# Optimization experiments

Hardware: AMD Instinct MI355X
Metric: run time of the kernel (lower is better)

Reference implementation:

```python
import jax, jax.numpy as jnp
import numpy as np

B, IN, X, OUT, Z = 4096, 1024, 2048, 512, 6
RES = [False, False, 1, False, 3, False]  # residual_in from init_kwargs
KEEP_P = 0.5  # y: Bernoulli keep-probability for connectivity mask


def _masked_normal(kw, km, shape):
    w = jax.random.normal(kw, shape, dtype=jnp.float32)
    m = jax.random.bernoulli(km, KEEP_P, shape).astype(jnp.float32)
    return w * m


def setup_inputs() -> dict:
    key = jax.random.key(0)
    ks = jax.random.split(key, 40)
    inp = {}
    inp['x'] = jax.random.normal(ks[0], (B, IN), dtype=jnp.float32)
    # weights stored as (in, out) == torch weight.T; mask baked in as in apply_connectivity()
    inp['W_in'] = _masked_normal(ks[1], ks[2], (IN, X))
    inp['b_in'] = jax.random.normal(ks[3], (X,), dtype=jnp.float32)
    hidden_in = [2 * X if RES[i] is not False else X for i in range(Z)]
    for i in range(Z):
        inp[f'Wh{i}'] = _masked_normal(ks[4 + 2 * i], ks[5 + 2 * i], (hidden_in[i], X))
    inp['bh'] = jax.random.normal(ks[20], (Z, X), dtype=jnp.float32)
    inp['W_out'] = _masked_normal(ks[21], ks[22], (X, OUT))
    inp['b_out'] = jax.random.normal(ks[23], (OUT,), dtype=jnp.float32)
    # per-column clip maxima: Poisson(rate=10) as in RandomActivation
    inp['mo_in'] = jax.random.poisson(ks[24], 10.0, (X,)).astype(jnp.float32)
    inp['mo_h'] = jax.random.poisson(ks[25], 10.0, (Z, X)).astype(jnp.float32)
    inp['mo_out'] = jax.random.poisson(ks[26], 10.0, (OUT,)).astype(jnp.float32)
    # per-column activation function ids in [0,5)
    inp['aid_in'] = jax.random.randint(ks[27], (X,), 0, 5, dtype=jnp.int32)
    inp['aid_h'] = jax.random.randint(ks[28], (Z, X), 0, 5, dtype=jnp.int32)
    inp['aid_out'] = jax.random.randint(ks[29], (OUT,), 0, 5, dtype=jnp.int32)
    return inp


def _rand_act(v, aid, mo):
    # fused per-column activation select (RandomActivation) + clip
    acts = [jax.nn.relu(v), jax.nn.sigmoid(v), jnp.tanh(v),
            jnp.where(v >= 0, v, 0.1 * v),  # LeakyReLU(0.1)
            jax.nn.selu(v)]
    out = jnp.select([aid == k for k in range(5)], acts, acts[0])
    return jnp.minimum(out, mo)


def reference(x, W_in, b_in, Wh0, Wh1, Wh2, Wh3, Wh4, Wh5, bh,
              W_out, b_out, mo_in, mo_h, mo_out, aid_in, aid_h, aid_out):
    Ws = [Wh0, Wh1, Wh2, Wh3, Wh4, Wh5]
    h = _rand_act(x @ W_in + b_in, aid_in, mo_in)
    outs = [h]  # temp_outputs
    for i in range(Z):
        if RES[i] is False:
            t = outs[i]
        else:
            t = jnp.concatenate([outs[i], outs[RES[i]]], axis=-1)
        outs.append(_rand_act(t @ Ws[i] + bh[i], aid_h[i], mo_h[i]))
    return _rand_act(outs[-1] @ W_out + b_out, aid_out, mo_out)
```

## Files before the change

### kernel.cpp

```cpp
#include <hip/hip_runtime.h>
#include <stdint.h>
#include <string.h>

#define BDIM   4096
#define INDIM  1024
#define XDIM   2048
#define OUTDIM 512
#define MCH    (BDIM / 16)

#define LO_SCALE 2048.0f
#define INV_LO_SCALE (1.0f / 2048.0f)

typedef _Float16 f16x8 __attribute__((ext_vector_type(8)));
typedef float f32x4 __attribute__((ext_vector_type(4)));
typedef unsigned short u16x8 __attribute__((ext_vector_type(8)));
typedef unsigned short u16x4 __attribute__((ext_vector_type(4)));

__device__ __forceinline__ unsigned short h2u(_Float16 h) {
  unsigned short u;
  memcpy(&u, &h, 2);
  return u;
}

__device__ __forceinline__ void split_h(float v, unsigned short& h,
                                        unsigned short& l) {
  _Float16 hh = (_Float16)v;
  float r = v - (float)hh;
  _Float16 ll = (_Float16)(r * LO_SCALE);
  h = h2u(hh);
  l = h2u(ll);
}

__device__ __forceinline__ void gld_lds16(const void* g, void* l) {
  __builtin_amdgcn_global_load_lds(
      (const __attribute__((address_space(1))) uint32_t*)g,
      (__attribute__((address_space(3))) uint32_t*)l, 16, 0, 0);
}

__device__ __forceinline__ float rand_act(float v, int a, float mo) {
  float r;
  if (a == 0) {
    r = fmaxf(v, 0.0f);
  } else if (a == 1) {
    r = 1.0f / (1.0f + expf(-v));
  } else if (a == 2) {
    r = tanhf(v);
  } else if (a == 3) {
    r = (v >= 0.0f) ? v : 0.1f * v;
  } else {
    r = (v > 0.0f) ? 1.0507009873554805f * v
                   : 1.7580993408473766f * expm1f(v);
  }
  return fminf(r, mo);
}


__global__ void pack_x(const float* __restrict__ s,
                       unsigned short* __restrict__ dh,
                       unsigned short* __restrict__ dl, int Kin) {
  int ks = blockIdx.x;
  int mblk = blockIdx.y;
  int cc = threadIdx.x >> 6;
  int lane = threadIdx.x & 63;
  int m16 = lane & 15, quad = lane >> 4;
  int row = mblk * 64 + cc * 16 + m16;
  const float* src = s + (size_t)row * Kin + ks * 32 + quad * 8;
  size_t o = ((size_t)ks * MCH + mblk * 4 + cc) * 512 + lane * 8;
  float4 v0 = *(const float4*)src;
  float4 v1 = *(const float4*)(src + 4);
  float vs[8] = {v0.x, v0.y, v0.z, v0.w, v1.x, v1.y, v1.z, v1.w};
  u16x8 vh, vl;
#pragma unroll
  for (int j = 0; j < 8; j++) {
    unsigned short h, l;
    split_h(vs[j], h, l);
    vh[j] = h;
    vl[j] = l;
  }
  *(u16x8*)(dh + o) = vh;
  *(u16x8*)(dl + o) = vl;
}

__global__ void pack_w(const float* __restrict__ W,
                       unsigned short* __restrict__ dh,
                       unsigned short* __restrict__ dl, int K, int N) {
  __shared__ float t[32][33];
  int n0 = blockIdx.x * 32, k0 = blockIdx.y * 32;
  int tx = threadIdx.x, ty = threadIdx.y;
#pragma unroll
  for (int i = 0; i < 32; i += 8)
    t[ty + i][tx] = W[(size_t)(k0 + ty + i) * N + n0 + tx];
  __syncthreads();
  int tt = ty * 32 + tx;
  int ci = tt >> 7;
  int rem = tt & 127;
  int lane = rem >> 1;
  int j4 = (rem & 1) * 4;
  int m16 = lane & 15, quad = lane >> 4;
  size_t o = ((size_t)(k0 >> 5) * (N >> 4) + (n0 >> 4) + ci) * 512 +
             lane * 8 + j4;
  u16x4 vh, vl;
#pragma unroll
  for (int jj = 0; jj < 4; jj++) {
    float v = t[quad * 8 + j4 + jj][ci * 16 + m16];
    unsigned short h, l;
    split_h(v, h, l);
    vh[jj] = h;
    vl[jj] = l;
  }
  *(u16x4*)(dh + o) = vh;
  *(u16x4*)(dl + o) = vl;
}

template <bool OUT_F16>
__global__ __launch_bounds__(256, 2) void gemm_split_act(
    const short* __restrict__ A1h, const short* __restrict__ A1l,
    const short* __restrict__ A2h, const short* __restrict__ A2l,
    const short* __restrict__ BTh, const short* __restrict__ BTl,
    const float* __restrict__ bias, const float* __restrict__ mo,
    const int* __restrict__ aid, unsigned short* __restrict__ Ch,
    unsigned short* __restrict__ Cl, float* __restrict__ Cf, int N, int K,
    int Ksplit) {
  __shared__ short lds0[8 * 512];
  __shared__ short lds1[8 * 512];
  __shared__ short lds2[8 * 512];

  const int tid = threadIdx.x;
  const int lane = tid & 63;
  const int wave = tid >> 6;
  const int m16 = lane & 15, quad = lane >> 4;

  const int nwg = gridDim.x * 64;
  const int lin = blockIdx.y * gridDim.x + blockIdx.x;
  const int cpx = nwg >> 3;
  const int virt = (lin & 7) * cpx + (lin >> 3);
  const int blockN = (virt >> 6) * 128;
  const int blockM = (virt & 63) * 64;

  f32x4 acc1[4][2];
  f32x4 acc2[4][2];
#pragma unroll
  for (int i = 0; i < 4; i++)
#pragma unroll
    for (int j = 0; j < 2; j++) {
      acc1[i][j] = (f32x4){0.f, 0.f, 0.f, 0.f};
      acc2[i][j] = (f32x4){0.f, 0.f, 0.f, 0.f};
    }

  const int KSTEPS = K >> 5;
  const int KS1 = Ksplit >> 5;

  const short* sAh = A1h;
  const short* sAl = A1l;
  const size_t aBase0 = (size_t)(blockM >> 4) * 512 + lane * 8;
  size_t aOff = aBase0;
  int stageK = 0;
  auto stageNext = [&](short* dst) {
#pragma unroll
    for (int s = 0; s < 2; s++) {
      int g = wave * 2 + s;
      const short* plane = (g < 4) ? sAh : sAl;
      gld_lds16(plane + aOff + (g & 3) * 512, dst + g * 512);
    }
    aOff += (size_t)MCH * 512;
    if (++stageK == KS1) { sAh = A2h; sAl = A2l; aOff = aBase0; }
  };

  size_t bOff = ((size_t)(blockN >> 4) + wave * 2) * 512 + lane * 8;
  const size_t bStride = (size_t)N * 32;
  auto loadBNext = [&](f16x8 (&bH)[2], f16x8 (&bL)[2]) {
    bH[0] = *(const f16x8*)(BTh + bOff);
    bH[1] = *(const f16x8*)(BTh + bOff + 512);
    bL[0] = *(const f16x8*)(BTl + bOff);
    bL[1] = *(const f16x8*)(BTl + bOff + 512);
    bOff += bStride;
  };

  f16x8 a0h[4], a0l[4], a1h[4], a1l[4];
  f16x8 b0H[2], b0L[2], b1H[2], b1L[2];

  auto ldsRead = [&](const short* src, f16x8 (&aH)[4], f16x8 (&aL)[4]) {
#pragma unroll
    for (int t = 0; t < 4; t++)
      aH[t] = *(const f16x8*)&src[t * 512 + lane * 8];
#pragma unroll
    for (int t = 0; t < 4; t++)
      aL[t] = *(const f16x8*)&src[(4 + t) * 512 + lane * 8];
  };

  auto ph12 = [&](f16x8 (&aH)[4], f16x8 (&bH)[2], f16x8 (&bL)[2]) {
    __builtin_amdgcn_s_setprio(1);
#pragma unroll
    for (int i = 0; i < 4; i++)
#pragma unroll
      for (int j = 0; j < 2; j++)
        acc1[i][j] = __builtin_amdgcn_mfma_f32_16x16x32_f16(aH[i], bH[j],
                                                            acc1[i][j], 0, 0, 0);
#pragma unroll
    for (int i = 0; i < 4; i++)
#pragma unroll
      for (int j = 0; j < 2; j++)
        acc2[i][j] = __builtin_amdgcn_mfma_f32_16x16x32_f16(aH[i], bL[j],
                                                            acc2[i][j], 0, 0, 0);
    __builtin_amdgcn_s_setprio(0);
  };
  auto ph3 = [&](f16x8 (&aL)[4], f16x8 (&bH)[2]) {
    __builtin_amdgcn_s_setprio(1);
#pragma unroll
    for (int i = 0; i < 4; i++)
#pragma unroll
      for (int j = 0; j < 2; j++)
        acc2[i][j] = __builtin_amdgcn_mfma_f32_16x16x32_f16(aL[i], bH[j],
                                                            acc2[i][j], 0, 0, 0);
    __builtin_amdgcn_s_setprio(0);
  };

#define SB0 __builtin_amdgcn_sched_barrier(0)

  auto ITER = [&](f16x8 (&aHc)[4], f16x8 (&aLc)[4], f16x8 (&aHn)[4],
                  f16x8 (&aLn)[4], f16x8 (&bHc)[2], f16x8 (&bLc)[2],
                  f16x8 (&bHn)[2], f16x8 (&bLn)[2], const short* src,
                  short* dst, bool doStage) {
    SB0;
    ph12(aHc, bHc, bLc);
    SB0;
    loadBNext(bHn, bLn);
    if (doStage) stageNext(dst);
    SB0;
    if (doStage)
      asm volatile("s_waitcnt vmcnt(6)" ::: "memory");
    else
      asm volatile("s_waitcnt vmcnt(4)" ::: "memory");
    __builtin_amdgcn_s_barrier();
    SB0;
    ldsRead(src, aHn, aLn);
    SB0;
    ph3(aLc, bHc);
    SB0;
  };

  stageNext(lds0);
  loadBNext(b0H, b0L);
  stageNext(lds1);
  asm volatile("s_waitcnt vmcnt(6)" ::: "memory");
  __builtin_amdgcn_s_barrier();
  SB0;
  ldsRead(lds0, a0h, a0l);

  short *bs = lds1, *bd = lds2, *bt = lds0;
  for (int ks = 0; ks <= KSTEPS - 4; ks += 2) {
    ITER(a0h, a0l, a1h, a1l, b0H, b0L, b1H, b1L, bs, bd, true);
    ITER(a1h, a1l, a0h, a0l, b1H, b1L, b0H, b0L, bd, bt, true);
    short* tmp = bs; bs = bt; bt = bd; bd = tmp;
  }
  ITER(a0h, a0l, a1h, a1l, b0H, b0L, b1H, b1L, bs, nullptr, false);
  SB0;
  ph12(a1h, b1H, b1L);
  ph3(a1l, b1H);

#pragma unroll
  for (int j = 0; j < 2; j++) {
    int col = blockN + wave * 32 + j * 16 + m16;
    float b = bias[col];
    float m = mo[col];
    int a = aid[col];
    size_t kbase = OUT_F16 ? ((size_t)(col >> 5) * MCH) * 512 +
                                 (size_t)((col >> 3) & 3) * 128 + (col & 7)
                           : 0;
#pragma unroll
    for (int i = 0; i < 4; i++) {
#pragma unroll
      for (int r = 0; r < 4; r++) {
        int row = blockM + i * 16 + quad * 4 + r;
        float s = acc1[i][j][r] + acc2[i][j][r] * INV_LO_SCALE;
        float v = rand_act(s + b, a, m);
        if (OUT_F16) {
          unsigned short h, l;
          split_h(v, h, l);
          size_t pidx = kbase + (size_t)(row >> 4) * 512 + (row & 15) * 8;
          Ch[pidx] = h;
          Cl[pidx] = l;
        } else {
          Cf[(size_t)row * N + col] = v;
        }
      }
    }
  }
}

extern "C" void kernel_launch(void* const* d_in, const int* in_sizes, int n_in,
                              void* d_out, int out_size, void* d_ws,
                              size_t ws_size, hipStream_t stream) {
  (void)in_sizes; (void)n_in; (void)out_size; (void)ws_size;

  const float* x     = (const float*)d_in[0];
  const float* W_in  = (const float*)d_in[1];
  const float* b_in  = (const float*)d_in[2];
  const float* Wh[6] = {(const float*)d_in[3], (const float*)d_in[4],
                        (const float*)d_in[5], (const float*)d_in[6],
                        (const float*)d_in[7], (const float*)d_in[8]};
  const float* bh    = (const float*)d_in[9];
  const float* W_out = (const float*)d_in[10];
  const float* b_out = (const float*)d_in[11];
  const float* mo_in = (const float*)d_in[12];
  const float* mo_h  = (const float*)d_in[13];
  const float* mo_out= (const float*)d_in[14];
  const int* aid_in  = (const int*)d_in[15];
  const int* aid_h   = (const int*)d_in[16];
  const int* aid_out = (const int*)d_in[17];

  const int hin[6] = {XDIM, XDIM, 2 * XDIM, XDIM, 2 * XDIM, XDIM};

  char* p = (char*)d_ws;
  auto take = [&](size_t elems) {
    short* q = (short*)p;
    p += elems * 2 * 2;
    return q;
  };
  short* x_s = take((size_t)BDIM * INDIM);
  size_t xpl = (size_t)BDIM * INDIM;
  short* w_in_s = take((size_t)XDIM * INDIM);
  size_t wpl_in = (size_t)XDIM * INDIM;
  short* w_h_s[6];
  size_t wpl_h[6];
  for (int i = 0; i < 6; i++) {
    wpl_h[i] = (size_t)XDIM * hin[i];
    w_h_s[i] = take(wpl_h[i]);
  }
  short* w_out_s = take((size_t)OUTDIM * XDIM);
  size_t wpl_out = (size_t)OUTDIM * XDIM;
  const size_t apl = (size_t)BDIM * XDIM;
  short* actA = take(apl);
  short* actB = take(apl);
  short* actC = take(apl);

  pack_x<<<dim3(INDIM / 32, BDIM / 64), dim3(256), 0, stream>>>(
      x, (unsigned short*)x_s, (unsigned short*)(x_s + xpl), INDIM);
  pack_w<<<dim3(XDIM / 32, INDIM / 32), dim3(32, 8), 0, stream>>>(
      W_in, (unsigned short*)w_in_s, (unsigned short*)(w_in_s + wpl_in), INDIM,
      XDIM);
  for (int i = 0; i < 6; i++)
    pack_w<<<dim3(XDIM / 32, hin[i] / 32), dim3(32, 8), 0, stream>>>(
        Wh[i], (unsigned short*)w_h_s[i],
        (unsigned short*)(w_h_s[i] + wpl_h[i]), hin[i], XDIM);
  pack_w<<<dim3(OUTDIM / 32, XDIM / 32), dim3(32, 8), 0, stream>>>(
      W_out, (unsigned short*)w_out_s, (unsigned short*)(w_out_s + wpl_out),
      XDIM, OUTDIM);

  auto G = [&](const short* A1, size_t a1pl, const short* A2, size_t a2pl,
               const short* W, size_t wpl, const float* bi, const float* m,
               const int* a, short* Cb, float* Cf, int N, int K, int Ks) {
    dim3 grid(N / 128, BDIM / 64);
    const short* A2h = A2;
    const short* A2l = A2 ? A2 + a2pl : nullptr;
    if (Cb)
      gemm_split_act<true><<<grid, 256, 0, stream>>>(
          A1, A1 + a1pl, A2h, A2l, W, W + wpl, bi, m, a, (unsigned short*)Cb,
          (unsigned short*)(Cb + apl), nullptr, N, K, Ks);
    else
      gemm_split_act<false><<<grid, 256, 0, stream>>>(
          A1, A1 + a1pl, A2h, A2l, W, W + wpl, bi, m, a, nullptr, nullptr, Cf,
          N, K, Ks);
  };

  G(x_s, xpl, nullptr, 0, w_in_s, wpl_in, b_in, mo_in, aid_in, actA, nullptr,
    XDIM, INDIM, INDIM);
  G(actA, apl, nullptr, 0, w_h_s[0], wpl_h[0], bh + 0 * XDIM, mo_h + 0 * XDIM,
    aid_h + 0 * XDIM, actB, nullptr, XDIM, XDIM, XDIM);
  G(actB, apl, nullptr, 0, w_h_s[1], wpl_h[1], bh + 1 * XDIM, mo_h + 1 * XDIM,
    aid_h + 1 * XDIM, actC, nullptr, XDIM, XDIM, XDIM);
  G(actC, apl, actB, apl, w_h_s[2], wpl_h[2], bh + 2 * XDIM, mo_h + 2 * XDIM,
    aid_h + 2 * XDIM, actA, nullptr, XDIM, 2 * XDIM, XDIM);
  G(actA, apl, nullptr, 0, w_h_s[3], wpl_h[3], bh + 3 * XDIM, mo_h + 3 * XDIM,
    aid_h + 3 * XDIM, actB, nullptr, XDIM, XDIM, XDIM);
  G(actB, apl, actA, apl, w_h_s[4], wpl_h[4], bh + 4 * XDIM, mo_h + 4 * XDIM,
    aid_h + 4 * XDIM, actC, nullptr, XDIM, 2 * XDIM, XDIM);
  G(actC, apl, nullptr, 0, w_h_s[5], wpl_h[5], bh + 5 * XDIM, mo_h + 5 * XDIM,
    aid_h + 5 * XDIM, actB, nullptr, XDIM, XDIM, XDIM);
  G(actB, apl, nullptr, 0, w_out_s, wpl_out, b_out, mo_out, aid_out, nullptr,
    (float*)d_out, OUTDIM, XDIM, XDIM);
}
```

Measured before the change: 1.352 ms.

## Drop A-fragment double buffering to fit three waves per SIMD and simplify tile mapping

```diff
diff --git a/kernel.cpp b/kernel.cpp
--- a/kernel.cpp
+++ b/kernel.cpp
@@ -113,7 +113,7 @@
 }
 
 template <bool OUT_F16>
-__global__ __launch_bounds__(256, 2) void gemm_split_act(
+__global__ __launch_bounds__(256, 3) void gemm_split_act(
     const short* __restrict__ A1h, const short* __restrict__ A1l,
     const short* __restrict__ A2h, const short* __restrict__ A2l,
     const short* __restrict__ BTh, const short* __restrict__ BTl,
@@ -130,12 +130,8 @@
   const int wave = tid >> 6;
   const int m16 = lane & 15, quad = lane >> 4;
 
-  const int nwg = gridDim.x * 64;
-  const int lin = blockIdx.y * gridDim.x + blockIdx.x;
-  const int cpx = nwg >> 3;
-  const int virt = (lin & 7) * cpx + (lin >> 3);
-  const int blockN = (virt >> 6) * 128;
-  const int blockM = (virt & 63) * 64;
+  const int blockN = blockIdx.x * 128;
+  const int blockM = blockIdx.y * 64;
 
   f32x4 acc1[4][2];
   f32x4 acc2[4][2];
@@ -176,10 +172,10 @@
     bOff += bStride;
   };
 
-  f16x8 a0h[4], a0l[4], a1h[4], a1l[4];
+  f16x8 aH[4], aL[4];
   f16x8 b0H[2], b0L[2], b1H[2], b1L[2];
 
-  auto ldsRead = [&](const short* src, f16x8 (&aH)[4], f16x8 (&aL)[4]) {
+  auto ldsRead = [&](const short* src) {
 #pragma unroll
     for (int t = 0; t < 4; t++)
       aH[t] = *(const f16x8*)&src[t * 512 + lane * 8];
@@ -188,7 +184,7 @@
       aL[t] = *(const f16x8*)&src[(4 + t) * 512 + lane * 8];
   };
 
-  auto ph12 = [&](f16x8 (&aH)[4], f16x8 (&bH)[2], f16x8 (&bL)[2]) {
+  auto ph12 = [&](f16x8 (&bH)[2], f16x8 (&bL)[2]) {
     __builtin_amdgcn_s_setprio(1);
 #pragma unroll
     for (int i = 0; i < 4; i++)
@@ -204,7 +200,7 @@
                                                             acc2[i][j], 0, 0, 0);
     __builtin_amdgcn_s_setprio(0);
   };
-  auto ph3 = [&](f16x8 (&aL)[4], f16x8 (&bH)[2]) {
+  auto ph3 = [&](f16x8 (&bH)[2]) {
     __builtin_amdgcn_s_setprio(1);
 #pragma unroll
     for (int i = 0; i < 4; i++)
@@ -216,28 +212,6 @@
   };
 
 #define SB0 __builtin_amdgcn_sched_barrier(0)
-
-  auto ITER = [&](f16x8 (&aHc)[4], f16x8 (&aLc)[4], f16x8 (&aHn)[4],
-                  f16x8 (&aLn)[4], f16x8 (&bHc)[2], f16x8 (&bLc)[2],
-                  f16x8 (&bHn)[2], f16x8 (&bLn)[2], const short* src,
-                  short* dst, bool doStage) {
-    SB0;
-    ph12(aHc, bHc, bLc);
-    SB0;
-    loadBNext(bHn, bLn);
-    if (doStage) stageNext(dst);
-    SB0;
-    if (doStage)
-      asm volatile("s_waitcnt vmcnt(6)" ::: "memory");
-    else
-      asm volatile("s_waitcnt vmcnt(4)" ::: "memory");
-    __builtin_amdgcn_s_barrier();
-    SB0;
-    ldsRead(src, aHn, aLn);
-    SB0;
-    ph3(aLc, bHc);
-    SB0;
-  };
 
   stageNext(lds0);
   loadBNext(b0H, b0L);
@@ -245,18 +219,53 @@
   asm volatile("s_waitcnt vmcnt(6)" ::: "memory");
   __builtin_amdgcn_s_barrier();
   SB0;
-  ldsRead(lds0, a0h, a0l);
-
-  short *bs = lds1, *bd = lds2, *bt = lds0;
+
+  short *p0 = lds0, *p1 = lds1, *p2 = lds2;
   for (int ks = 0; ks <= KSTEPS - 4; ks += 2) {
-    ITER(a0h, a0l, a1h, a1l, b0H, b0L, b1H, b1L, bs, bd, true);
-    ITER(a1h, a1l, a0h, a0l, b1H, b1L, b0H, b0L, bd, bt, true);
-    short* tmp = bs; bs = bt; bt = bd; bd = tmp;
-  }
-  ITER(a0h, a0l, a1h, a1l, b0H, b0L, b1H, b1L, bs, nullptr, false);
-  SB0;
-  ph12(a1h, b1H, b1L);
-  ph3(a1l, b1H);
+    ldsRead(p0);
+    loadBNext(b1H, b1L);
+    stageNext(p2);
+    SB0;
+    asm volatile("s_waitcnt vmcnt(8)" ::: "memory");
+    SB0;
+    ph12(b0H, b0L);
+    ph3(b0H);
+    SB0;
+    asm volatile("s_waitcnt vmcnt(6)" ::: "memory");
+    __builtin_amdgcn_s_barrier();
+    SB0;
+    ldsRead(p1);
+    loadBNext(b0H, b0L);
+    stageNext(p0);
+    SB0;
+    asm volatile("s_waitcnt vmcnt(8)" ::: "memory");
+    SB0;
+    ph12(b1H, b1L);
+    ph3(b1H);
+    SB0;
+    asm volatile("s_waitcnt vmcnt(6)" ::: "memory");
+    __builtin_amdgcn_s_barrier();
+    SB0;
+    short* t = p0; p0 = p2; p2 = p1; p1 = t;
+  }
+
+  ldsRead(p0);
+  loadBNext(b1H, b1L);
+  SB0;
+  asm volatile("s_waitcnt vmcnt(6)" ::: "memory");
+  SB0;
+  ph12(b0H, b0L);
+  ph3(b0H);
+  SB0;
+  asm volatile("s_waitcnt vmcnt(4)" ::: "memory");
+  __builtin_amdgcn_s_barrier();
+  SB0;
+  ldsRead(p1);
+  SB0;
+  asm volatile("s_waitcnt vmcnt(0)" ::: "memory");
+  SB0;
+  ph12(b1H, b1L);
+  ph3(b1H);
 
 #pragma unroll
   for (int j = 0; j < 2; j++) {
```

New measurement: 1.225 ms. 9.3% less time.
